# Kernel optimization log

Hardware: AMD Instinct MI355X
Metric: run time of the kernel (lower is better)

## Reference

```python
import jax, jax.numpy as jnp
import numpy as np

B, S, D, H, E, K = 4, 2048, 1024, 512, 64, 8


def setup_inputs() -> dict:
    key = jax.random.key(0)
    k1, k2, k3, k4 = jax.random.split(key, 4)
    x = jax.random.normal(k1, (B, S, D), dtype=jnp.float32)
    # gate weight stored as [D, E] (equivalent to torch Linear weight [E, D] transposed)
    Wg = jax.random.normal(k2, (D, E), dtype=jnp.float32) * (1.0 / np.sqrt(D))
    Wup = jax.random.normal(k3, (E, D, H), dtype=jnp.float32) * (1.0 / np.sqrt(D))
    Wdown = jax.random.normal(k4, (E, H, D), dtype=jnp.float32) * (1.0 / np.sqrt(H))
    return {"x": x, "Wg": Wg, "Wup": Wup, "Wdown": Wdown}


def reference(x, Wg, Wup, Wdown):
    # NOTE: ExpertMLP.forward in the source ignores gate_proj: out = down(silu(up(x)))
    T = B * S
    flat = x.reshape(T, D)                        # [T, D]
    logits = flat @ Wg                            # [T, E]
    topk_scores, topk_idx = jax.lax.top_k(logits, K)   # [T, K]
    gate_w = jax.nn.softmax(topk_scores, axis=-1)       # [T, K]
    # dense combine matrix [T, E]; topk indices are unique per token
    rows = jnp.arange(T)[:, None]
    combine = jnp.zeros((T, E), dtype=x.dtype).at[rows, topk_idx].set(gate_w)
    # scan over experts: each expert runs on all tokens, masked/weighted by combine
    def body(acc, params):
        wu, wd, c = params                         # [D,H], [H,D], [T]
        h = jax.nn.silu(flat @ wu)                 # [T, H]
        y = h @ wd                                 # [T, D]
        return acc + c[:, None] * y, None
    out0 = jnp.zeros((T, D), dtype=x.dtype)
    out, _ = jax.lax.scan(body, out0, (Wup, Wdown, combine.T))
    return out.reshape(B, S, D)
```

## Files before the change

### kernel.cpp

```cpp
#include <hip/hip_runtime.h>
#include <hip/hip_bf16.h>
#include <stdint.h>
#include <math.h>

#define T_TOK 8192
#define DDIM  1024
#define HDIM  512
#define NEXP  64
#define TOPK  8
#define CHUNKS 16

typedef __bf16 bf16x8 __attribute__((ext_vector_type(8)));
typedef float  f32x4  __attribute__((ext_vector_type(4)));

__device__ __forceinline__ void load_lds16(const void* gp, void* lp){
  __builtin_amdgcn_global_load_lds(
      (__attribute__((address_space(1))) void*)(uintptr_t)gp,
      (__attribute__((address_space(3))) void*)lp, 16, 0, 0);
}

__device__ __forceinline__ unsigned short f2bfbits(float f){
  union { __bf16 b; unsigned short u; } cv; cv.b = (__bf16)f; return cv.u;
}
__device__ __forceinline__ float bf2f(unsigned short s){
  unsigned int u = ((unsigned int)s) << 16; return __uint_as_float(u);
}

__global__ __launch_bounds__(256) void k_transpose_cvt64(const float* __restrict__ src,
                                                         __bf16* __restrict__ dst,
                                                         int R, int C){
  __shared__ float tile[64][65];
  const int z  = blockIdx.z;
  const int c0 = blockIdx.x * 64;
  const int r0 = blockIdx.y * 64;
  const float* s = src + (size_t)z * R * C;
  __bf16*      d = dst + (size_t)z * R * C;
  const int t = threadIdx.x;
  const int rrow = t >> 4, rchunk = t & 15;
  #pragma unroll
  for (int rep = 0; rep < 4; rep++){
    int r = rrow + (rep << 4);
    float4 v = *(const float4*)(s + (size_t)(r0 + r) * C + c0 + (rchunk << 2));
    tile[(rchunk << 2) + 0][r] = v.x;
    tile[(rchunk << 2) + 1][r] = v.y;
    tile[(rchunk << 2) + 2][r] = v.z;
    tile[(rchunk << 2) + 3][r] = v.w;
  }
  __syncthreads();
  const int wc = t >> 3, wj = t & 7;
  #pragma unroll
  for (int rep = 0; rep < 2; rep++){
    int c = wc + (rep << 5);
    bf16x8 o;
    #pragma unroll
    for (int sidx = 0; sidx < 8; sidx++)
      o[sidx] = (__bf16)tile[c][(wj << 3) + sidx];
    *(bf16x8*)(d + (size_t)(c0 + c) * R + r0 + (wj << 3)) = o;
  }
}

__global__ __launch_bounds__(256) void k_gate(const float* __restrict__ x,
                                              const float* __restrict__ Wg,
                                              float* __restrict__ logits,
                                              __bf16* __restrict__ xb){
  __shared__ float xs[32][64];
  __shared__ float ws[32][64];
  const int tid = threadIdx.x;
  const int m0  = blockIdx.x * 64;
  const int tm  = (tid >> 4) << 2;
  const int tn  = (tid & 15) << 2;
  const int sr  = tid >> 2;
  const int sc  = tid & 3;
  double acc[4][4];
  #pragma unroll
  for (int i=0;i<4;i++)
    #pragma unroll
    for (int j=0;j<4;j++) acc[i][j]=0.0;

  for (int k0 = 0; k0 < DDIM; k0 += 32){
    {
      const float4* g = (const float4*)(Wg + (size_t)k0 * 64);
      float4* l = (float4*)&ws[0][0];
      l[tid]       = g[tid];
      l[tid + 256] = g[tid + 256];
    }
    {
      const float* g = x + (size_t)(m0 + sr) * DDIM + k0 + sc * 8;
      float4 a = *(const float4*)g;
      float4 b = *(const float4*)(g + 4);
      xs[sc*8+0][sr]=a.x; xs[sc*8+1][sr]=a.y; xs[sc*8+2][sr]=a.z; xs[sc*8+3][sr]=a.w;
      xs[sc*8+4][sr]=b.x; xs[sc*8+5][sr]=b.y; xs[sc*8+6][sr]=b.z; xs[sc*8+7][sr]=b.w;
      bf16x8 o;
      o[0]=(__bf16)a.x; o[1]=(__bf16)a.y; o[2]=(__bf16)a.z; o[3]=(__bf16)a.w;
      o[4]=(__bf16)b.x; o[5]=(__bf16)b.y; o[6]=(__bf16)b.z; o[7]=(__bf16)b.w;
      *(bf16x8*)(xb + (size_t)(m0 + sr) * DDIM + k0 + sc * 8) = o;
    }
    __syncthreads();
    for (int k = 0; k < 32; k++){
      float4 a4 = *(const float4*)&xs[k][tm];
      float4 b4 = *(const float4*)&ws[k][tn];
      float av[4] = {a4.x,a4.y,a4.z,a4.w};
      float bv[4] = {b4.x,b4.y,b4.z,b4.w};
      #pragma unroll
      for (int i=0;i<4;i++)
        #pragma unroll
        for (int j=0;j<4;j++)
          acc[i][j] += (double)av[i] * (double)bv[j];
    }
    __syncthreads();
  }
  #pragma unroll
  for (int i=0;i<4;i++){
    float4 o = make_float4((float)acc[i][0],(float)acc[i][1],(float)acc[i][2],(float)acc[i][3]);
    *(float4*)&logits[(size_t)(m0 + tm + i) * 64 + tn] = o;
  }
}

__global__ __launch_bounds__(256) void k_topk(const float* __restrict__ logits,
                                              int* __restrict__ tk_idx,
                                              float* __restrict__ tk_w){
  const int lane = threadIdx.x & 63;
  const int t    = blockIdx.x * 4 + (threadIdx.x >> 6);
  float v = logits[(size_t)t * 64 + lane];
  const int myi = lane;
  float mv[8]; int mi[8];
  #pragma unroll
  for (int k = 0; k < 8; k++){
    float bv = v; int bi = myi;
    #pragma unroll
    for (int off = 32; off > 0; off >>= 1){
      float ov = __shfl_xor(bv, off, 64);
      int   oi = __shfl_xor(bi, off, 64);
      if (ov > bv || (ov == bv && oi < bi)){ bv = ov; bi = oi; }
    }
    mv[k] = bv; mi[k] = bi;
    if (bi == myi) v = -INFINITY;
  }
  float w[8]; float s = 0.f;
  #pragma unroll
  for (int k = 0; k < 8; k++){ w[k] = expf(mv[k] - mv[0]); s += w[k]; }
  float inv = 1.0f / s;
  if (lane == 0){
    #pragma unroll
    for (int k = 0; k < 8; k++){
      tk_idx[(size_t)t * 8 + k] = mi[k];
      tk_w [(size_t)t * 8 + k] = w[k] * inv;
    }
  }
}

__global__ __launch_bounds__(256) void k_hist(const int* __restrict__ tk_idx,
                                              int* __restrict__ g_hist){
  __shared__ int h[4][64];
  const int tid = threadIdx.x, wave = tid >> 6;
  ((int*)h)[tid] = 0;
  __syncthreads();
  const int4* p = (const int4*)(tk_idx + blockIdx.x * 4096);
  #pragma unroll
  for (int i = 0; i < 4; i++){
    int4 v = p[i * 256 + tid];
    atomicAdd(&h[wave][v.x], 1); atomicAdd(&h[wave][v.y], 1);
    atomicAdd(&h[wave][v.z], 1); atomicAdd(&h[wave][v.w], 1);
  }
  __syncthreads();
  if (tid < 64)
    g_hist[blockIdx.x * 64 + tid] = h[0][tid] + h[1][tid] + h[2][tid] + h[3][tid];
}

__global__ void k_scan(const int* __restrict__ g_hist,
                       int* __restrict__ offsets,
                       int* __restrict__ g_base){
  const int e = threadIdx.x;
  int h[CHUNKS]; int tot = 0;
  #pragma unroll
  for (int c = 0; c < CHUNKS; c++){ h[c] = g_hist[c * 64 + e]; tot += h[c]; }
  int inc = tot;
  #pragma unroll
  for (int off = 1; off < 64; off <<= 1){
    int n = __shfl_up(inc, off, 64);
    if (e >= off) inc += n;
  }
  int exc = inc - tot;
  offsets[e] = exc;
  if (e == 63) offsets[64] = inc;
  int b = exc;
  #pragma unroll
  for (int c = 0; c < CHUNKS; c++){ g_base[c * 64 + e] = b; b += h[c]; }
}

__global__ __launch_bounds__(256) void k_scatter(const int* __restrict__ tk_idx,
                                                 const int* __restrict__ g_base,
                                                 int* __restrict__ slot_token,
                                                 int* __restrict__ inv_pos){
  __shared__ int cnt[64];
  const int tid = threadIdx.x;
  if (tid < 64) cnt[tid] = g_base[blockIdx.x * 64 + tid];
  __syncthreads();
  const int base = blockIdx.x * 4096;
  #pragma unroll
  for (int i = 0; i < 16; i++){
    int gid = base + i * 256 + tid;
    int e = tk_idx[gid];
    int pos = atomicAdd(&cnt[e], 1);
    slot_token[pos] = gid >> 3;
    inv_pos[gid] = pos;
  }
}

__global__ __launch_bounds__(256, 4) void k_gemm1(const __bf16* __restrict__ xb,
                                                  const __bf16* __restrict__ wupT,
                                                  const int* __restrict__ offsets,
                                                  const int* __restrict__ slot_token,
                                                  __bf16* __restrict__ h){
  const int bid = blockIdx.x;
  const int L   = ((bid & 7) << 8) | (bid >> 3);
  const int e   = L >> 5;
  const int mb  = L & 7;
  const int nb  = (L >> 3) & 3;
  const int base = offsets[e];
  const int ne   = offsets[e + 1] - base;
  const int n0   = nb << 7;

  __shared__ __align__(16) __bf16 As[2][128 * 32];
  __shared__ __align__(16) __bf16 Bs[2][128 * 32];
  __shared__ int s_tok[128];

  const int tid = threadIdx.x;
  const int wave = tid >> 6, lane = tid & 63;
  const int wm = (wave >> 1) << 6;
  const int wn = (wave & 1) << 6;
  const int fr = lane & 15, kc = lane >> 4;
  const int rxor = (fr & 3) ^ ((fr >> 2) & 3);
  const __bf16* wB = wupT + (size_t)e * HDIM * DDIM + (size_t)n0 * DDIM;

  const int srl  = lane >> 2;
  const int sxor = (srl & 3) ^ ((srl >> 2) & 3);
  const int scol = ((lane & 3) ^ sxor) << 3;
  const __bf16* gB[2]; int ldsOff[2];
  #pragma unroll
  for (int q = 0; q < 2; q++){
    int r = (q << 6) + (wave << 4) + srl;
    gB[q] = wB + (size_t)r * DDIM + scol;
    ldsOff[q] = (q << 11) + (wave << 9);
  }

  const int cr = (lane >> 4) << 2, cc = lane & 15;

  for (int m0 = mb << 7; m0 < ne; m0 += 1024){
    __syncthreads();
    if (tid < 128){
      int r = m0 + tid;
      s_tok[tid] = slot_token[base + (r < ne ? r : (ne - 1))];
    }
    __syncthreads();

    const __bf16* gA[2];
    #pragma unroll
    for (int q = 0; q < 2; q++)
      gA[q] = xb + (size_t)s_tok[(q << 6) + (wave << 4) + srl] * DDIM + scol;

    f32x4 acc[4][4];
    #pragma unroll
    for (int i=0;i<4;i++)
      #pragma unroll
      for (int j=0;j<4;j++) acc[i][j] = (f32x4){0.f,0.f,0.f,0.f};

    #pragma unroll
    for (int q = 0; q < 2; q++){
      load_lds16(gA[q], (void*)&As[0][ldsOff[q]]);
      load_lds16(gB[q], (void*)&Bs[0][ldsOff[q]]);
    }
    __syncthreads();

    const int NK = DDIM / 32;
    for (int t = 0; t < NK; ++t){
      const int cur = t & 1;
      if (t + 1 < NK){
        const int k1 = (t + 1) << 5;
        const int nxt = cur ^ 1;
        #pragma unroll
        for (int q = 0; q < 2; q++){
          load_lds16(gA[q] + k1, (void*)&As[nxt][ldsOff[q]]);
          load_lds16(gB[q] + k1, (void*)&Bs[nxt][ldsOff[q]]);
        }
      }
      const int cA = (kc ^ rxor) << 3;
      bf16x8 af[4], bg[4];
      #pragma unroll
      for (int i=0;i<4;i++) af[i] = *(const bf16x8*)&As[cur][((wm + (i<<4) + fr) << 5) + cA];
      #pragma unroll
      for (int j=0;j<4;j++) bg[j] = *(const bf16x8*)&Bs[cur][((wn + (j<<4) + fr) << 5) + cA];
      #pragma unroll
      for (int i=0;i<4;i++)
        #pragma unroll
        for (int j=0;j<4;j++)
          acc[i][j] = __builtin_amdgcn_mfma_f32_16x16x32_bf16(af[i], bg[j], acc[i][j], 0, 0, 0);
      __syncthreads();
    }

    #pragma unroll
    for (int i=0;i<4;i++){
      #pragma unroll
      for (int reg=0;reg<4;reg++){
        int rl = wm + (i << 4) + cr + reg;
        int gm = m0 + rl;
        if (gm < ne){
          __bf16* hrow = h + (size_t)(base + gm) * HDIM + n0 + wn;
          #pragma unroll
          for (int j=0;j<4;j++){
            float v  = acc[i][j][reg];
            float sv = v / (1.0f + __expf(-v));
            unsigned short u = f2bfbits(sv);
            int part = __shfl_xor((int)u, 1, 64);
            if (!(lane & 1)){
              unsigned int packed = ((unsigned int)(unsigned short)part << 16) | u;
              *(unsigned int*)((unsigned short*)hrow + (j << 4) + cc) = packed;
            }
          }
        }
      }
    }
  }
}

__global__ __launch_bounds__(256, 2) void k_gemm2(const __bf16* __restrict__ h,
                                                  const __bf16* __restrict__ wdownT,
                                                  const int* __restrict__ offsets,
                                                  __bf16* __restrict__ y,
                                                  int elo){
  const int bid = blockIdx.x;
  const int L   = ((bid & 7) << 8) | (bid >> 3);
  const int e   = elo + (L >> 6);
  const int mb  = L & 7;
  const int nb  = (L >> 3) & 7;
  const int base = offsets[e];
  const int ne   = offsets[e + 1] - base;
  const int n0   = nb << 7;
  const int ybase = offsets[elo];

  __shared__ __align__(16) __bf16 As[2][128 * 64];
  __shared__ __align__(16) __bf16 Bs[2][128 * 64];

  const int tid = threadIdx.x;
  const int wave = tid >> 6, lane = tid & 63;
  const int wm = (wave >> 1) << 6;
  const int wn = (wave & 1) << 6;
  const int fr = lane & 15, kc = lane >> 4;
  const int rxor = fr & 7;
  const __bf16* wB = wdownT + (size_t)e * DDIM * HDIM + (size_t)n0 * HDIM;

  const int srl  = lane >> 3;
  const int scol = ((lane & 7) ^ srl) << 3;
  const __bf16* gB[4]; int ldsOff[4];
  #pragma unroll
  for (int q = 0; q < 4; q++){
    int r = (wave << 5) + (q << 3) + srl;
    gB[q] = wB + (size_t)r * HDIM + scol;
    ldsOff[q] = ((wave << 5) + (q << 3)) << 6;
  }

  const int cr = (lane >> 4) << 2, cc = lane & 15;

  for (int m0 = mb << 7; m0 < ne; m0 += 1024){
    const __bf16* gA[4];
    #pragma unroll
    for (int q = 0; q < 4; q++){
      int sl = m0 + (wave << 5) + (q << 3) + srl; if (sl >= ne) sl = ne - 1;
      gA[q] = h + (size_t)(base + sl) * HDIM + scol;
    }

    f32x4 acc[4][4];
    #pragma unroll
    for (int i=0;i<4;i++)
      #pragma unroll
      for (int j=0;j<4;j++) acc[i][j] = (f32x4){0.f,0.f,0.f,0.f};

    __syncthreads();
    #pragma unroll
    for (int q = 0; q < 4; q++){
      load_lds16(gA[q], (void*)&As[0][ldsOff[q]]);
      load_lds16(gB[q], (void*)&Bs[0][ldsOff[q]]);
    }
    __syncthreads();

    const int NK = HDIM / 64;
    for (int t = 0; t < NK; ++t){
      const int cur = t & 1;
      if (t + 1 < NK){
        const int k1 = (t + 1) << 6;
        const int nxt = cur ^ 1;
        #pragma unroll
        for (int q = 0; q < 4; q++){
          load_lds16(gA[q] + k1, (void*)&As[nxt][ldsOff[q]]);
          load_lds16(gB[q] + k1, (void*)&Bs[nxt][ldsOff[q]]);
        }
      }
      #pragma unroll
      for (int ks = 0; ks < 2; ks++){
        const int cA = (((ks << 2) + kc) ^ rxor) << 3;
        bf16x8 af[4], bg[4];
        #pragma unroll
        for (int i=0;i<4;i++) af[i] = *(const bf16x8*)&As[cur][((wm + (i<<4) + fr) << 6) + cA];
        #pragma unroll
        for (int j=0;j<4;j++) bg[j] = *(const bf16x8*)&Bs[cur][((wn + (j<<4) + fr) << 6) + cA];
        #pragma unroll
        for (int i=0;i<4;i++)
          #pragma unroll
          for (int j=0;j<4;j++)
            acc[i][j] = __builtin_amdgcn_mfma_f32_16x16x32_bf16(af[i], bg[j], acc[i][j], 0, 0, 0);
      }
      __syncthreads();
    }

    #pragma unroll
    for (int i=0;i<4;i++){
      #pragma unroll
      for (int reg=0;reg<4;reg++){
        int rl = wm + (i << 4) + cr + reg;
        int gm = m0 + rl;
        if (gm < ne){
          __bf16* yrow = y + (size_t)(base - ybase + gm) * DDIM + n0 + wn;
          #pragma unroll
          for (int j=0;j<4;j++){
            unsigned short u = f2bfbits(acc[i][j][reg]);
            int part = __shfl_xor((int)u, 1, 64);
            if (!(lane & 1)){
              unsigned int packed = ((unsigned int)(unsigned short)part << 16) | u;
              *(unsigned int*)((unsigned short*)yrow + (j << 4) + cc) = packed;
            }
          }
        }
      }
    }
  }
}

__global__ __launch_bounds__(256) void k_combine(const __bf16* __restrict__ y,
                                                 const int* __restrict__ tk_idx,
                                                 const float* __restrict__ tk_w,
                                                 const int* __restrict__ inv_pos,
                                                 const int* __restrict__ offsets,
                                                 float* __restrict__ out,
                                                 int elo, int ehi, int first){
  const int t   = blockIdx.x;
  const int tid = threadIdx.x;
  __shared__ int se[8]; __shared__ float sw[8]; __shared__ int sp[8];
  if (tid < 8){
    se[tid] = tk_idx[(size_t)t * 8 + tid];
    sw[tid] = tk_w [(size_t)t * 8 + tid];
    sp[tid] = inv_pos[(size_t)t * 8 + tid];
  }
  __syncthreads();
  const int ybase = offsets[elo];
  const int c = tid << 2;
  float4 acc;
  if (first) acc = make_float4(0.f, 0.f, 0.f, 0.f);
  else       acc = *(const float4*)&out[(size_t)t * DDIM + c];
  #pragma unroll
  for (int k = 0; k < 8; k++){
    int e = se[k];
    if (e >= elo && e < ehi){
      const unsigned short* yr = (const unsigned short*)y + (size_t)(sp[k] - ybase) * DDIM + c;
      ushort4 raw = *(const ushort4*)yr;
      float w = sw[k];
      acc.x += w * bf2f(raw.x);
      acc.y += w * bf2f(raw.y);
      acc.z += w * bf2f(raw.z);
      acc.w += w * bf2f(raw.w);
    }
  }
  *(float4*)&out[(size_t)t * DDIM + c] = acc;
}

extern "C" void kernel_launch(void* const* d_in, const int* in_sizes, int n_in,
                              void* d_out, int out_size, void* d_ws, size_t ws_size,
                              hipStream_t stream){
  const float* x     = (const float*)d_in[0];
  const float* Wg    = (const float*)d_in[1];
  const float* Wup   = (const float*)d_in[2];
  const float* Wdown = (const float*)d_in[3];
  float* out = (float*)d_out;

  char* ws = (char*)d_ws;
  size_t off = 0;
  auto alloc = [&](size_t bytes) -> void* {
    void* p = ws + off;
    off += (bytes + 255) & ~(size_t)255;
    return p;
  };
  __bf16* wupT      = (__bf16*)alloc((size_t)NEXP * DDIM * HDIM * 2);
  __bf16* xb        = (__bf16*)alloc((size_t)T_TOK * DDIM * 2);
  float*  logits    = (float*)alloc((size_t)T_TOK * NEXP * 4);
  __bf16* wdownT    = (__bf16*)alloc((size_t)NEXP * DDIM * HDIM * 2);
  __bf16* hbuf      = (__bf16*)alloc((size_t)T_TOK * TOPK * HDIM * 2);
  int*    tk_idx    = (int*)  alloc((size_t)T_TOK * TOPK * 4);
  float*  tk_w      = (float*)alloc((size_t)T_TOK * TOPK * 4);
  int*    slot_tok  = (int*)  alloc((size_t)T_TOK * TOPK * 4);
  int*    inv_pos   = (int*)  alloc((size_t)T_TOK * TOPK * 4);
  int*    g_hist    = (int*)  alloc((size_t)CHUNKS * 64 * 4);
  int*    g_base    = (int*)  alloc((size_t)CHUNKS * 64 * 4);
  int*    offsets   = (int*)  alloc(512);
  __bf16* ybuf      = (__bf16*)ws;

  k_gate<<<T_TOK / 64, 256, 0, stream>>>(x, Wg, logits, xb);
  k_transpose_cvt64<<<dim3(DDIM/64, HDIM/64, 64), 256, 0, stream>>>(Wdown, wdownT, HDIM, DDIM);
  k_transpose_cvt64<<<dim3(HDIM/64, DDIM/64, 64), 256, 0, stream>>>(Wup,   wupT,   DDIM, HDIM);
  k_topk<<<T_TOK / 4, 256, 0, stream>>>(logits, tk_idx, tk_w);
  k_hist<<<CHUNKS, 256, 0, stream>>>(tk_idx, g_hist);
  k_scan<<<1, 64, 0, stream>>>(g_hist, offsets, g_base);
  k_scatter<<<CHUNKS, 256, 0, stream>>>(tk_idx, g_base, slot_tok, inv_pos);
  k_gemm1<<<2048, 256, 0, stream>>>(xb, wupT, offsets, slot_tok, hbuf);
  k_gemm2<<<2048, 256, 0, stream>>>(hbuf, wdownT, offsets, ybuf, 0);
  k_combine<<<T_TOK, 256, 0, stream>>>(ybuf, tk_idx, tk_w, inv_pos, offsets, out, 0, 32, 1);
  k_gemm2<<<2048, 256, 0, stream>>>(hbuf, wdownT, offsets, ybuf, 32);
  k_combine<<<T_TOK, 256, 0, stream>>>(ybuf, tk_idx, tk_w, inv_pos, offsets, out, 32, 64, 0);
}
```

Baseline: 575.5 us.

## Widen gemm1 tile to 128x256 with 8 waves and merge weight transposes

The up-projection GEMM now uses 512-thread blocks with a 128x256 output tile, halving the block count so each gathered A tile of token rows is reused across twice as many output columns, and doubling the B shared-memory buffer. The two weight transpose/convert launches are merged into one kernel that picks the source tensor from the block index, saving a launch. The larger tile raises LDS use to about 48KB per block and changes occupancy, and the launch-bound hint asks for 6 blocks per CU, which may not be reachable.

```diff
diff --git a/kernel.cpp b/kernel.cpp
--- a/kernel.cpp
+++ b/kernel.cpp
@@ -26,13 +26,23 @@
   unsigned int u = ((unsigned int)s) << 16; return __uint_as_float(u);
 }
 
-__global__ __launch_bounds__(256) void k_transpose_cvt64(const float* __restrict__ src,
-                                                         __bf16* __restrict__ dst,
-                                                         int R, int C){
+__global__ __launch_bounds__(256) void k_transpose_both(const float* __restrict__ Wdown,
+                                                        const float* __restrict__ Wup,
+                                                        __bf16* __restrict__ wdownT,
+                                                        __bf16* __restrict__ wupT){
   __shared__ float tile[64][65];
-  const int z  = blockIdx.z;
-  const int c0 = blockIdx.x * 64;
-  const int r0 = blockIdx.y * 64;
+  const int b = blockIdx.x;
+  const float* src; __bf16* dst; int R, C, c0, r0, z;
+  if (b < 8192){
+    z = b >> 7; int tt = b & 127;
+    c0 = (tt & 15) << 6; r0 = (tt >> 4) << 6;
+    src = Wdown; dst = wdownT; R = HDIM; C = DDIM;
+  } else {
+    int bb = b - 8192;
+    z = bb >> 7; int tt = bb & 127;
+    c0 = (tt & 7) << 6; r0 = (tt >> 3) << 6;
+    src = Wup; dst = wupT; R = DDIM; C = HDIM;
+  }
   const float* s = src + (size_t)z * R * C;
   __bf16*      d = dst + (size_t)z * R * C;
   const int t = threadIdx.x;
@@ -207,28 +217,28 @@
   }
 }
 
-__global__ __launch_bounds__(256, 4) void k_gemm1(const __bf16* __restrict__ xb,
+__global__ __launch_bounds__(512, 6) void k_gemm1(const __bf16* __restrict__ xb,
                                                   const __bf16* __restrict__ wupT,
                                                   const int* __restrict__ offsets,
                                                   const int* __restrict__ slot_token,
                                                   __bf16* __restrict__ h){
   const int bid = blockIdx.x;
-  const int L   = ((bid & 7) << 8) | (bid >> 3);
-  const int e   = L >> 5;
+  const int L   = ((bid & 7) << 7) | (bid >> 3);
+  const int e   = L >> 4;
   const int mb  = L & 7;
-  const int nb  = (L >> 3) & 3;
+  const int nb  = (L >> 3) & 1;
   const int base = offsets[e];
   const int ne   = offsets[e + 1] - base;
-  const int n0   = nb << 7;
+  const int n0   = nb << 8;
 
   __shared__ __align__(16) __bf16 As[2][128 * 32];
-  __shared__ __align__(16) __bf16 Bs[2][128 * 32];
+  __shared__ __align__(16) __bf16 Bs[2][256 * 32];
   __shared__ int s_tok[128];
 
   const int tid = threadIdx.x;
   const int wave = tid >> 6, lane = tid & 63;
-  const int wm = (wave >> 1) << 6;
-  const int wn = (wave & 1) << 6;
+  const int wm = (wave >> 2) << 6;
+  const int wn = (wave & 3) << 6;
   const int fr = lane & 15, kc = lane >> 4;
   const int rxor = (fr & 3) ^ ((fr >> 2) & 3);
   const __bf16* wB = wupT + (size_t)e * HDIM * DDIM + (size_t)n0 * DDIM;
@@ -236,12 +246,13 @@
   const int srl  = lane >> 2;
   const int sxor = (srl & 3) ^ ((srl >> 2) & 3);
   const int scol = ((lane & 3) ^ sxor) << 3;
-  const __bf16* gB[2]; int ldsOff[2];
+  const int arow = (wave << 4) + srl;
+  const int aOff = wave << 9;
+  const __bf16* gB[2]; int bOff[2];
   #pragma unroll
   for (int q = 0; q < 2; q++){
-    int r = (q << 6) + (wave << 4) + srl;
-    gB[q] = wB + (size_t)r * DDIM + scol;
-    ldsOff[q] = (q << 11) + (wave << 9);
+    gB[q] = wB + (size_t)((q << 7) + arow) * DDIM + scol;
+    bOff[q] = (q << 12) + (wave << 9);
   }
 
   const int cr = (lane >> 4) << 2, cc = lane & 15;
@@ -254,10 +265,7 @@
     }
     __syncthreads();
 
-    const __bf16* gA[2];
-    #pragma unroll
-    for (int q = 0; q < 2; q++)
-      gA[q] = xb + (size_t)s_tok[(q << 6) + (wave << 4) + srl] * DDIM + scol;
+    const __bf16* gA = xb + (size_t)s_tok[arow] * DDIM + scol;
 
     f32x4 acc[4][4];
     #pragma unroll
@@ -265,11 +273,9 @@
       #pragma unroll
       for (int j=0;j<4;j++) acc[i][j] = (f32x4){0.f,0.f,0.f,0.f};
 
-    #pragma unroll
-    for (int q = 0; q < 2; q++){
-      load_lds16(gA[q], (void*)&As[0][ldsOff[q]]);
-      load_lds16(gB[q], (void*)&Bs[0][ldsOff[q]]);
-    }
+    load_lds16(gA, (void*)&As[0][aOff]);
+    load_lds16(gB[0], (void*)&Bs[0][bOff[0]]);
+    load_lds16(gB[1], (void*)&Bs[0][bOff[1]]);
     __syncthreads();
 
     const int NK = DDIM / 32;
@@ -278,11 +284,9 @@
       if (t + 1 < NK){
         const int k1 = (t + 1) << 5;
         const int nxt = cur ^ 1;
-        #pragma unroll
-        for (int q = 0; q < 2; q++){
-          load_lds16(gA[q] + k1, (void*)&As[nxt][ldsOff[q]]);
-          load_lds16(gB[q] + k1, (void*)&Bs[nxt][ldsOff[q]]);
-        }
+        load_lds16(gA + k1, (void*)&As[nxt][aOff]);
+        load_lds16(gB[0] + k1, (void*)&Bs[nxt][bOff[0]]);
+        load_lds16(gB[1] + k1, (void*)&Bs[nxt][bOff[1]]);
       }
       const int cA = (kc ^ rxor) << 3;
       bf16x8 af[4], bg[4];
@@ -503,13 +507,12 @@
   __bf16* ybuf      = (__bf16*)ws;
 
   k_gate<<<T_TOK / 64, 256, 0, stream>>>(x, Wg, logits, xb);
-  k_transpose_cvt64<<<dim3(DDIM/64, HDIM/64, 64), 256, 0, stream>>>(Wdown, wdownT, HDIM, DDIM);
-  k_transpose_cvt64<<<dim3(HDIM/64, DDIM/64, 64), 256, 0, stream>>>(Wup,   wupT,   DDIM, HDIM);
+  k_transpose_both<<<16384, 256, 0, stream>>>(Wdown, Wup, wdownT, wupT);
   k_topk<<<T_TOK / 4, 256, 0, stream>>>(logits, tk_idx, tk_w);
   k_hist<<<CHUNKS, 256, 0, stream>>>(tk_idx, g_hist);
   k_scan<<<1, 64, 0, stream>>>(g_hist, offsets, g_base);
   k_scatter<<<CHUNKS, 256, 0, stream>>>(tk_idx, g_base, slot_tok, inv_pos);
-  k_gemm1<<<2048, 256, 0, stream>>>(xb, wupT, offsets, slot_tok, hbuf);
+  k_gemm1<<<1024, 512, 0, stream>>>(xb, wupT, offsets, slot_tok, hbuf);
   k_gemm2<<<2048, 256, 0, stream>>>(hbuf, wdownT, offsets, ybuf, 0);
   k_combine<<<T_TOK, 256, 0, stream>>>(ybuf, tk_idx, tk_w, inv_pos, offsets, out, 0, 32, 1);
   k_gemm2<<<2048, 256, 0, stream>>>(hbuf, wdownT, offsets, ybuf, 32);
```

Measured after the change: 835.8 us. +45.2%, slower.
